# Kernel tuning notes

Hardware: AMD Instinct MI355X
Metric: run time of the kernel (lower is better)

## Reference

```python
import jax, jax.numpy as jnp
import numpy as np

N, D, K = 32768, 128, 16
EPS = 1e-8  # torch cosine_similarity eps


def setup_inputs() -> dict:
    key = jax.random.key(0)
    k1, k2, kW1, kW2, kV = jax.random.split(key, 5)
    # xavier_normal std for [K, fan_in, fan_out]-style tensors (torch treats dim0 as batch? no:
    # xavier_normal_ on a 3D tensor uses fan_in = D*1? torch computes fan from dims 1.. with receptive field.
    # fan_in = size(1)*rf, fan_out = size(0)*rf where rf = prod(shape[2:]).
    def xavier_std(shape):
        rf = int(np.prod(shape[2:])) if len(shape) > 2 else 1
        fan_in = shape[1] * rf
        fan_out = shape[0] * rf
        return float(np.sqrt(2.0 / (fan_in + fan_out)))
    W1 = jax.random.normal(kW1, (K, D, D), jnp.float32) * xavier_std((K, D, D))
    W2 = jax.random.normal(kW2, (K, D, D), jnp.float32) * xavier_std((K, D, D))
    V = jax.random.normal(kV, (K, 2 * D, 1), jnp.float32) * xavier_std((K, 2 * D, 1))
    b = jnp.zeros((K,), jnp.float32)
    x_1 = jax.random.normal(k1, (N, D), jnp.float32)
    x_2 = jax.random.normal(k2, (N, D), jnp.float32)
    return {"x_1": x_1, "x_2": x_2, "W1": W1, "W2": W2, "V": V, "b": b}


def reference(x_1, x_2, W1, W2, V, b):
    # Batched version of the per-slice loop: one bmm per side instead of K matmuls.
    x1_t = jnp.einsum('nd,kde->kne', x_1, W1)  # [K, N, D]
    x2_t = jnp.einsum('nd,kde->kne', x_2, W2)  # [K, N, D]
    # torch.cosine_similarity(dim=-1): dot / (clamp(||a||, eps) * clamp(||b||, eps))
    num = jnp.sum(x1_t * x2_t, axis=-1)                      # [K, N]
    n1 = jnp.maximum(jnp.sqrt(jnp.sum(x1_t * x1_t, -1)), EPS)
    n2 = jnp.maximum(jnp.sqrt(jnp.sum(x2_t * x2_t, -1)), EPS)
    part1 = num / (n1 * n2)                                  # [K, N]
    x_cat = jnp.concatenate([x_1, x_2], axis=-1)             # [N, 2D]
    part2 = jnp.einsum('nc,kc->kn', x_cat, V[:, :, 0])       # [K, N]
    fea = part1 + part2 + b[:, None]                         # [K, N]
    return jax.nn.relu(fea.T)                                # [N, K]
```

## Files before the change

kernel.cpp:

```cpp
#include <hip/hip_runtime.h>


typedef __attribute__((ext_vector_type(8))) __bf16 bf16x8;
typedef __attribute__((ext_vector_type(8))) unsigned short us8;
typedef __attribute__((ext_vector_type(4))) float f32x4;

static __device__ __forceinline__ unsigned short f2bf(float f) {
  unsigned u = __float_as_uint(f);
  u += 0x7FFFu + ((u >> 16) & 1u);
  return (unsigned short)(u >> 16);
}

static __device__ __forceinline__ bf16x8 as_bf(us8 u) {
  bf16x8 r;
  __builtin_memcpy(&r, &u, sizeof(r));
  return r;
}

__global__ void ntn_prep_w(const float* __restrict__ W1, const float* __restrict__ W2,
                           unsigned short* __restrict__ wsW) {
  __shared__ float T[128 * 68];
  const int t = threadIdx.x;
  const int blk = blockIdx.x;
  const int k = blk >> 2, side = (blk >> 1) & 1, h = blk & 1;
  const float* W = (side ? W2 : W1) + k * 16384 + h * 64;

#pragma unroll
  for (int i = 0; i < 8; ++i) {
    int fidx = i * 256 + t;
    int d = fidx >> 4, c4 = fidx & 15;
    float4 v = *(const float4*)(W + d * 128 + c4 * 4);
    *(float4*)&T[d * 68 + c4 * 4] = v;
  }
  __syncthreads();

  const size_t base = ((size_t)(k * 2 + h) * 2048 + side * 1024) * 8;
#pragma unroll
  for (int ui = 0; ui < 4; ++ui) {
    int u = ui * 256 + t;
    int lane = u & 63, s = (u >> 6) & 3, et2 = (u >> 8) & 3;
    int q = lane >> 4, l15 = lane & 15;
    int d0 = s * 32 + q * 8, e = et2 * 16 + l15;
    us8 r;
#pragma unroll
    for (int j = 0; j < 8; ++j) r[j] = f2bf(T[(d0 + j) * 68 + e]);
    *(us8*)(wsW + base + (size_t)u * 8) = r;
  }
}

__global__ void ntn_prep_v(const float* __restrict__ V, unsigned short* __restrict__ wsV) {
  int u = blockIdx.x * 256 + threadIdx.x;
  if (u < 512) {
    int lane = u & 63, cs = u >> 6;
    int q = lane >> 4, l15 = lane & 15;
    const float* src = V + l15 * 256 + cs * 32 + q * 8;
    us8 r;
#pragma unroll
    for (int j = 0; j < 8; ++j) r[j] = f2bf(src[j]);
    *(us8*)(wsV + (size_t)u * 8) = r;
  }
}

__global__ __launch_bounds__(256, 2) void ntn_main(
    const float* __restrict__ x1, const float* __restrict__ x2,
    const float* __restrict__ b,
    const unsigned short* __restrict__ wsW, const unsigned short* __restrict__ wsV,
    float* __restrict__ out) {
  __shared__ uint4 ldsW[2][2048];

  const int tid = threadIdx.x;
  const int lane = tid & 63, wave = tid >> 6;
  const int q = lane >> 4, l15 = lane & 15;
  const int kh = blockIdx.x & 3;
  const int rb = blockIdx.x >> 2;
  const int rowbase = rb * 256 + wave * 64;

  const f32x4 zero4 = {0.f, 0.f, 0.f, 0.f};

  auto stage = [&](int cc, int slot) {
    const unsigned short* src = wsW + (size_t)cc * 16384 + (size_t)(wave * 512 + lane) * 8;
    uint4* dst = &ldsW[slot][wave * 512];
#pragma unroll
    for (int i = 0; i < 8; ++i)
      __builtin_amdgcn_global_load_lds(
          (__attribute__((address_space(1))) void*)(void*)(src + i * 512),
          (__attribute__((address_space(3))) void*)(dst + i * 64), 16, 0, 0);
  };

  stage(kh * 8, 0);

  bf16x8 xb[2][4][4];
#pragma unroll
  for (int side = 0; side < 2; ++side) {
    const float* xp0 = side ? x2 : x1;
#pragma unroll
    for (int nt = 0; nt < 4; ++nt) {
#pragma unroll
      for (int s = 0; s < 4; ++s) {
        const float* p = xp0 + (size_t)(rowbase + nt * 16 + l15) * 128 + s * 32 + q * 8;
        float4 v0 = *(const float4*)p;
        float4 v1 = *(const float4*)(p + 4);
        us8 uu;
        uu[0] = f2bf(v0.x); uu[1] = f2bf(v0.y); uu[2] = f2bf(v0.z); uu[3] = f2bf(v0.w);
        uu[4] = f2bf(v1.x); uu[5] = f2bf(v1.y); uu[6] = f2bf(v1.z); uu[7] = f2bf(v1.w);
        xb[side][nt][s] = as_bf(uu);
      }
    }
  }

  f32x4 accP[4];
  {
    float4 bv = *(const float4*)(b + q * 4);
#pragma unroll
    for (int nt = 0; nt < 4; ++nt) {
      f32x4 a = zero4;
#pragma unroll
      for (int cs = 0; cs < 8; ++cs) {
        bf16x8 vf = as_bf(*(const us8*)(wsV + (size_t)(cs * 64 + lane) * 8));
        a = __builtin_amdgcn_mfma_f32_16x16x32_bf16(vf, xb[cs >> 2][nt][cs & 3], a, 0, 0, 0);
      }
      a.x += bv.x; a.y += bv.y; a.z += bv.z; a.w += bv.w;
      accP[nt] = a;
    }
  }

  float nm[4] = {0.f, 0.f, 0.f, 0.f};
  float q1[4] = {0.f, 0.f, 0.f, 0.f};
  float q2[4] = {0.f, 0.f, 0.f, 0.f};

  auto compute = [&](int slot) {
#pragma unroll
    for (int et = 0; et < 4; ++et) {
      bf16x8 wa[4], wb[4];
#pragma unroll
      for (int s = 0; s < 4; ++s) {
        wa[s] = as_bf(*(const us8*)&ldsW[slot][et * 256 + s * 64 + lane]);
        wb[s] = as_bf(*(const us8*)&ldsW[slot][1024 + et * 256 + s * 64 + lane]);
      }
#pragma unroll
      for (int nt = 0; nt < 4; ++nt) {
        f32x4 a1 = zero4, a2 = zero4;
#pragma unroll
        for (int s = 0; s < 4; ++s)
          a1 = __builtin_amdgcn_mfma_f32_16x16x32_bf16(wa[s], xb[0][nt][s], a1, 0, 0, 0);
#pragma unroll
        for (int s = 0; s < 4; ++s)
          a2 = __builtin_amdgcn_mfma_f32_16x16x32_bf16(wb[s], xb[1][nt][s], a2, 0, 0, 0);
        nm[nt] += a1.x * a2.x + a1.y * a2.y + a1.z * a2.z + a1.w * a2.w;
        q1[nt] += a1.x * a1.x + a1.y * a1.y + a1.z * a1.z + a1.w * a1.w;
        q2[nt] += a2.x * a2.x + a2.y * a2.y + a2.z * a2.z + a2.w * a2.w;
      }
    }
  };

#pragma unroll
  for (int kk = 0; kk < 4; ++kk) {
    const int cbase = kh * 8 + 2 * kk;
    __syncthreads();
    stage(cbase + 1, 1);
    compute(0);
    __syncthreads();
    if (kk < 3) stage(cbase + 2, 0);
    compute(1);

#pragma unroll
    for (int nt = 0; nt < 4; ++nt) {
      float n = nm[nt], s1 = q1[nt], s2 = q2[nt];
      n  += __shfl_xor(n, 16);  n  += __shfl_xor(n, 32);
      s1 += __shfl_xor(s1, 16); s1 += __shfl_xor(s1, 32);
      s2 += __shfl_xor(s2, 16); s2 += __shfl_xor(s2, 32);
      float d1 = fmaxf(sqrtf(s1), 1e-8f);
      float d2 = fmaxf(sqrtf(s2), 1e-8f);
      float p1 = n / (d1 * d2);
      if (kk == 0)      accP[nt].x = fmaxf(accP[nt].x + p1, 0.f);
      else if (kk == 1) accP[nt].y = fmaxf(accP[nt].y + p1, 0.f);
      else if (kk == 2) accP[nt].z = fmaxf(accP[nt].z + p1, 0.f);
      else              accP[nt].w = fmaxf(accP[nt].w + p1, 0.f);
      nm[nt] = 0.f; q1[nt] = 0.f; q2[nt] = 0.f;
    }
  }

  if (q == kh) {
#pragma unroll
    for (int nt = 0; nt < 4; ++nt)
      *(f32x4*)(out + (size_t)(rowbase + nt * 16 + l15) * 16 + kh * 4) = accP[nt];
  }
}

extern "C" void kernel_launch(void* const* d_in, const int* in_sizes, int n_in,
                              void* d_out, int out_size, void* d_ws, size_t ws_size,
                              hipStream_t stream) {
  const float* x1 = (const float*)d_in[0];
  const float* x2 = (const float*)d_in[1];
  const float* W1 = (const float*)d_in[2];
  const float* W2 = (const float*)d_in[3];
  const float* V  = (const float*)d_in[4];
  const float* b  = (const float*)d_in[5];
  float* out = (float*)d_out;
  unsigned short* wsW = (unsigned short*)d_ws;
  unsigned short* wsV = wsW + (size_t)65536 * 8;

  ntn_prep_w<<<64, 256, 0, stream>>>(W1, W2, wsW);
  ntn_prep_v<<<2, 256, 0, stream>>>(V, wsV);
  ntn_main<<<512, 256, 0, stream>>>(x1, x2, b, wsW, wsV, out);
}
```

Before: 144.8 us.

## Halve rows per block, shrink W chunks, raise occupancy and merge prep kernels

Each main-kernel block now covers 128 rows instead of 256, and each wave holds 32 rows, so there are twice as many blocks. W is staged in half-size chunks (16 pipelined chunks per block), which halves LDS use and register footprint and allows launch bounds of 4 blocks per CU. The K loop is no longer unrolled, and outputs are written as scalars per k instead of one vector store at the end. The two prep kernels are merged into one launch. The trade-off is more barriers, more x reloads overall and scattered scalar stores.

```diff
diff --git a/kernel.cpp b/kernel.cpp
--- a/kernel.cpp
+++ b/kernel.cpp
@@ -17,11 +17,29 @@
   return r;
 }
 
-__global__ void ntn_prep_w(const float* __restrict__ W1, const float* __restrict__ W2,
-                           unsigned short* __restrict__ wsW) {
-  __shared__ float T[128 * 68];
+__global__ void ntn_prep(const float* __restrict__ W1, const float* __restrict__ W2,
+                         const float* __restrict__ V,
+                         unsigned short* __restrict__ wsW, unsigned short* __restrict__ wsV) {
   const int t = threadIdx.x;
   const int blk = blockIdx.x;
+  if (blk == 64) {
+    if (t < 128) {
+#pragma unroll
+      for (int ui = 0; ui < 4; ++ui) {
+        int u = ui * 128 + t;
+        int lane = u & 63, cs = u >> 6;
+        int q = lane >> 4, l15 = lane & 15;
+        const float* src = V + l15 * 256 + cs * 32 + q * 8;
+        us8 r;
+#pragma unroll
+        for (int j = 0; j < 8; ++j) r[j] = f2bf(src[j]);
+        *(us8*)(wsV + (size_t)u * 8) = r;
+      }
+    }
+    return;
+  }
+
+  __shared__ float T[128 * 68];
   const int k = blk >> 2, side = (blk >> 1) & 1, h = blk & 1;
   const float* W = (side ? W2 : W1) + k * 16384 + h * 64;
 
@@ -34,67 +52,57 @@
   }
   __syncthreads();
 
-  const size_t base = ((size_t)(k * 2 + h) * 2048 + side * 1024) * 8;
 #pragma unroll
   for (int ui = 0; ui < 4; ++ui) {
     int u = ui * 256 + t;
-    int lane = u & 63, s = (u >> 6) & 3, et2 = (u >> 8) & 3;
+    int lane = u & 63, s = (u >> 6) & 3, et2f = (u >> 8) & 3;
     int q = lane >> 4, l15 = lane & 15;
-    int d0 = s * 32 + q * 8, e = et2 * 16 + l15;
+    int d0 = s * 32 + q * 8;
+    int el = et2f * 16 + l15;
     us8 r;
 #pragma unroll
-    for (int j = 0; j < 8; ++j) r[j] = f2bf(T[(d0 + j) * 68 + e]);
-    *(us8*)(wsW + base + (size_t)u * 8) = r;
-  }
-}
-
-__global__ void ntn_prep_v(const float* __restrict__ V, unsigned short* __restrict__ wsV) {
-  int u = blockIdx.x * 256 + threadIdx.x;
-  if (u < 512) {
-    int lane = u & 63, cs = u >> 6;
-    int q = lane >> 4, l15 = lane & 15;
-    const float* src = V + l15 * 256 + cs * 32 + q * 8;
-    us8 r;
-#pragma unroll
-    for (int j = 0; j < 8; ++j) r[j] = f2bf(src[j]);
-    *(us8*)(wsV + (size_t)u * 8) = r;
-  }
-}
-
-__global__ __launch_bounds__(256, 2) void ntn_main(
+    for (int j = 0; j < 8; ++j) r[j] = f2bf(T[(d0 + j) * 68 + el]);
+    int cc = k * 4 + h * 2 + (et2f >> 1);
+    int uic = side * 512 + (et2f & 1) * 256 + s * 64 + lane;
+    *(us8*)(wsW + ((size_t)cc * 1024 + uic) * 8) = r;
+  }
+}
+
+__global__ __launch_bounds__(256, 4) void ntn_main(
     const float* __restrict__ x1, const float* __restrict__ x2,
     const float* __restrict__ b,
     const unsigned short* __restrict__ wsW, const unsigned short* __restrict__ wsV,
     float* __restrict__ out) {
-  __shared__ uint4 ldsW[2][2048];
+  __shared__ uint4 ldsW[2][1024];
 
   const int tid = threadIdx.x;
   const int lane = tid & 63, wave = tid >> 6;
   const int q = lane >> 4, l15 = lane & 15;
   const int kh = blockIdx.x & 3;
   const int rb = blockIdx.x >> 2;
-  const int rowbase = rb * 256 + wave * 64;
+  const int rowbase = rb * 128 + wave * 32;
 
   const f32x4 zero4 = {0.f, 0.f, 0.f, 0.f};
 
   auto stage = [&](int cc, int slot) {
-    const unsigned short* src = wsW + (size_t)cc * 16384 + (size_t)(wave * 512 + lane) * 8;
-    uint4* dst = &ldsW[slot][wave * 512];
-#pragma unroll
-    for (int i = 0; i < 8; ++i)
+    const unsigned short* src = wsW + (size_t)cc * 8192 + (size_t)(wave * 256 + lane) * 8;
+    uint4* dst = &ldsW[slot][wave * 256];
+#pragma unroll
+    for (int i = 0; i < 4; ++i)
       __builtin_amdgcn_global_load_lds(
           (__attribute__((address_space(1))) void*)(void*)(src + i * 512),
           (__attribute__((address_space(3))) void*)(dst + i * 64), 16, 0, 0);
   };
 
-  stage(kh * 8, 0);
-
-  bf16x8 xb[2][4][4];
+  const int cbase = kh * 16;
+  stage(cbase, 0);
+
+  bf16x8 xb[2][2][4];
 #pragma unroll
   for (int side = 0; side < 2; ++side) {
     const float* xp0 = side ? x2 : x1;
 #pragma unroll
-    for (int nt = 0; nt < 4; ++nt) {
+    for (int nt = 0; nt < 2; ++nt) {
 #pragma unroll
       for (int s = 0; s < 4; ++s) {
         const float* p = xp0 + (size_t)(rowbase + nt * 16 + l15) * 128 + s * 32 + q * 8;
@@ -108,11 +116,11 @@
     }
   }
 
-  f32x4 accP[4];
+  f32x4 accP[2];
   {
     float4 bv = *(const float4*)(b + q * 4);
 #pragma unroll
-    for (int nt = 0; nt < 4; ++nt) {
+    for (int nt = 0; nt < 2; ++nt) {
       f32x4 a = zero4;
 #pragma unroll
       for (int cs = 0; cs < 8; ++cs) {
@@ -124,21 +132,19 @@
     }
   }
 
-  float nm[4] = {0.f, 0.f, 0.f, 0.f};
-  float q1[4] = {0.f, 0.f, 0.f, 0.f};
-  float q2[4] = {0.f, 0.f, 0.f, 0.f};
+  float nm[2] = {0.f, 0.f}, q1[2] = {0.f, 0.f}, q2[2] = {0.f, 0.f};
 
   auto compute = [&](int slot) {
 #pragma unroll
-    for (int et = 0; et < 4; ++et) {
+    for (int et = 0; et < 2; ++et) {
       bf16x8 wa[4], wb[4];
 #pragma unroll
       for (int s = 0; s < 4; ++s) {
         wa[s] = as_bf(*(const us8*)&ldsW[slot][et * 256 + s * 64 + lane]);
-        wb[s] = as_bf(*(const us8*)&ldsW[slot][1024 + et * 256 + s * 64 + lane]);
-      }
-#pragma unroll
-      for (int nt = 0; nt < 4; ++nt) {
+        wb[s] = as_bf(*(const us8*)&ldsW[slot][512 + et * 256 + s * 64 + lane]);
+      }
+#pragma unroll
+      for (int nt = 0; nt < 2; ++nt) {
         f32x4 a1 = zero4, a2 = zero4;
 #pragma unroll
         for (int s = 0; s < 4; ++s)
@@ -153,18 +159,19 @@
     }
   };
 
-#pragma unroll
+#pragma unroll 1
   for (int kk = 0; kk < 4; ++kk) {
-    const int cbase = kh * 8 + 2 * kk;
-    __syncthreads();
-    stage(cbase + 1, 1);
-    compute(0);
-    __syncthreads();
-    if (kk < 3) stage(cbase + 2, 0);
-    compute(1);
-
-#pragma unroll
-    for (int nt = 0; nt < 4; ++nt) {
+#pragma unroll
+    for (int q4 = 0; q4 < 4; ++q4) {
+      const int c = kk * 4 + q4;
+      __syncthreads();
+      if (c < 15) stage(cbase + c + 1, (c + 1) & 1);
+      compute(c & 1);
+    }
+
+    const int k = kh * 4 + kk;
+#pragma unroll
+    for (int nt = 0; nt < 2; ++nt) {
       float n = nm[nt], s1 = q1[nt], s2 = q2[nt];
       n  += __shfl_xor(n, 16);  n  += __shfl_xor(n, 32);
       s1 += __shfl_xor(s1, 16); s1 += __shfl_xor(s1, 32);
@@ -172,18 +179,12 @@
       float d1 = fmaxf(sqrtf(s1), 1e-8f);
       float d2 = fmaxf(sqrtf(s2), 1e-8f);
       float p1 = n / (d1 * d2);
-      if (kk == 0)      accP[nt].x = fmaxf(accP[nt].x + p1, 0.f);
-      else if (kk == 1) accP[nt].y = fmaxf(accP[nt].y + p1, 0.f);
-      else if (kk == 2) accP[nt].z = fmaxf(accP[nt].z + p1, 0.f);
-      else              accP[nt].w = fmaxf(accP[nt].w + p1, 0.f);
+      float pc = (kk == 0) ? accP[nt].x : (kk == 1) ? accP[nt].y
+               : (kk == 2) ? accP[nt].z : accP[nt].w;
+      if (q == kh)
+        out[(size_t)(rowbase + nt * 16 + l15) * 16 + k] = fmaxf(p1 + pc, 0.f);
       nm[nt] = 0.f; q1[nt] = 0.f; q2[nt] = 0.f;
     }
-  }
-
-  if (q == kh) {
-#pragma unroll
-    for (int nt = 0; nt < 4; ++nt)
-      *(f32x4*)(out + (size_t)(rowbase + nt * 16 + l15) * 16 + kh * 4) = accP[nt];
   }
 }
 
@@ -200,7 +201,6 @@
   unsigned short* wsW = (unsigned short*)d_ws;
   unsigned short* wsV = wsW + (size_t)65536 * 8;
 
-  ntn_prep_w<<<64, 256, 0, stream>>>(W1, W2, wsW);
-  ntn_prep_v<<<2, 256, 0, stream>>>(V, wsV);
-  ntn_main<<<512, 256, 0, stream>>>(x1, x2, b, wsW, wsV, out);
-}
+  ntn_prep<<<65, 256, 0, stream>>>(W1, W2, V, wsW, wsV);
+  ntn_main<<<1024, 256, 0, stream>>>(x1, x2, b, wsW, wsV, out);
+}
```

Result: slower. 249.6 us (+72.4%).
